# Performance work log

Hardware: AMD Instinct MI355X
Metric: run time of the kernel (lower is better)

Reference implementation:

```python
import jax, jax.numpy as jnp
import numpy as np

NINP = 768
HEAD = 12
ATTN_DIM = 768
PROT_DIM = 1024
B, T, S = 4, 2048, 512
EPS = 1e-5


def _lin_params(key, d_in, d_out):
    k1, k2 = jax.random.split(key)
    lim = 1.0 / np.sqrt(d_in)
    W = jax.random.uniform(k1, (d_in, d_out), jnp.float32, -lim, lim)
    b = jax.random.uniform(k2, (d_out,), jnp.float32, -lim, lim)
    return W, b


def setup_inputs() -> dict:
    key = jax.random.key(0)
    ks = jax.random.split(key, 16)
    x = jax.random.normal(ks[0], (B, T, NINP), jnp.float32)
    enc = jax.random.normal(ks[1], (B, S, PROT_DIM), jnp.float32)
    sWq, sbq = _lin_params(ks[2], NINP, ATTN_DIM)
    sWk, sbk = _lin_params(ks[3], NINP, ATTN_DIM)
    sWv, sbv = _lin_params(ks[4], NINP, ATTN_DIM)
    sWo, sbo = _lin_params(ks[5], ATTN_DIM, NINP)
    cWq, cbq = _lin_params(ks[6], NINP, ATTN_DIM)
    cWk, cbk = _lin_params(ks[7], PROT_DIM, ATTN_DIM)
    cWv, cbv = _lin_params(ks[8], PROT_DIM, ATTN_DIM)
    cWo, cbo = _lin_params(ks[9], ATTN_DIM, NINP)
    mW1, mb1 = _lin_params(ks[10], NINP, 4 * NINP)
    mW2, mb2 = _lin_params(ks[11], 4 * NINP, NINP)
    return dict(
        x=x, encoder_hidden_states=enc,
        ln1_g=jnp.ones((NINP,)), ln1_b=jnp.zeros((NINP,)),
        ln2_g=jnp.ones((NINP,)), ln2_b=jnp.zeros((NINP,)),
        sWq=sWq, sbq=sbq, sWk=sWk, sbk=sbk, sWv=sWv, sbv=sbv, sWo=sWo, sbo=sbo,
        cWq=cWq, cbq=cbq, cWk=cWk, cbk=cbk, cWv=cWv, cbv=cbv, cWo=cWo, cbo=cbo,
        mW1=mW1, mb1=mb1, mW2=mW2, mb2=mb2,
    )


def _ln(x, g, b):
    mu = jnp.mean(x, -1, keepdims=True)
    var = jnp.mean(jnp.square(x - mu), -1, keepdims=True)
    return (x - mu) * jax.lax.rsqrt(var + EPS) * g + b


def _attn(xq, xkv, Wq, bq, Wk, bk, Wv, bv, Wo, bo, causal):
    Bq, Tq, _ = xq.shape
    Sk = xkv.shape[1]
    hd = ATTN_DIM // HEAD
    q = (xq @ Wq + bq).reshape(Bq, Tq, HEAD, hd).transpose(0, 2, 1, 3)
    k = (xkv @ Wk + bk).reshape(Bq, Sk, HEAD, hd).transpose(0, 2, 1, 3)
    v = (xkv @ Wv + bv).reshape(Bq, Sk, HEAD, hd).transpose(0, 2, 1, 3)
    att = jnp.einsum('bhtd,bhsd->bhts', q, k) * (1.0 / np.sqrt(hd))
    if causal:
        mask = jnp.tril(jnp.ones((Tq, Sk), bool))
        att = jnp.where(mask, att, -jnp.inf)
    att = jax.nn.softmax(att, axis=-1)
    y = jnp.einsum('bhts,bhsd->bhtd', att, v)
    y = y.transpose(0, 2, 1, 3).reshape(Bq, Tq, ATTN_DIM)
    return y @ Wo + bo


def reference(x, encoder_hidden_states, ln1_g, ln1_b, ln2_g, ln2_b,
              sWq, sbq, sWk, sbk, sWv, sbv, sWo, sbo,
              cWq, cbq, cWk, cbk, cWv, cbv, cWo, cbo,
              mW1, mb1, mW2, mb2):
    # NOTE: original code does x = ln1(x), so the residual adds onto the
    # NORMED input (faithful to source quirk). is_causal=True, multi_mode=True.
    xn = _ln(x, ln1_g, ln1_b)
    x = xn + _attn(xn, xn, sWq, sbq, sWk, sbk, sWv, sbv, sWo, sbo, causal=True)
    x = x + _attn(x, encoder_hidden_states, cWq, cbq, cWk, cbk, cWv, cbv, cWo, cbo, causal=False)
    h = _ln(x, ln2_g, ln2_b)
    h = jax.nn.gelu(h @ mW1 + mb1, approximate=False) @ mW2 + mb2
    return x + h
```

## Files before the change

kernel.cpp:

```cpp
#include <hip/hip_runtime.h>
#include <math.h>

typedef unsigned short u16;
typedef __attribute__((ext_vector_type(8))) short short8;
typedef __attribute__((ext_vector_type(4))) short bf16x4;
typedef __attribute__((ext_vector_type(4))) float f32x4;

static __device__ __forceinline__ u16 f2bf(float f) {
    union { float f; unsigned int u; } c; c.f = f;
    unsigned int u = c.u;
    u += 0x7FFF + ((u >> 16) & 1);
    return (u16)(u >> 16);
}
static __device__ __forceinline__ float bf2f(u16 u) {
    union { unsigned int i; float f; } c; c.i = ((unsigned int)u) << 16;
    return c.f;
}
static __device__ __forceinline__ float gelu_f(float v) {
    float y = 0.7978845608f * (v + 0.044715f * v * v * v);
    return v / (1.0f + __expf(-2.0f * y));
}

#define GLOAD16(g, s) __builtin_amdgcn_global_load_lds( \
    (const __attribute__((address_space(1))) void*)(g), \
    (__attribute__((address_space(3))) void*)(s), 16, 0, 0)

struct PrepArgs {
    const float* src[11];
    u16* dst[11];
    int K[11];
    int N[11];
    int end[11];
    int cnt;
};

__global__ void k_prep(PrepArgs a)
{
    __shared__ float tile[32][33];
    const int bid = blockIdx.x;
    int e = 0;
    while (e < a.cnt - 1 && bid >= a.end[e]) e++;
    const int local = bid - (e ? a.end[e - 1] : 0);
    const float* __restrict__ src = a.src[e];
    u16* __restrict__ dst = a.dst[e];
    const int K = a.K[e], N = a.N[e];
    const int tx = threadIdx.x, ty = threadIdx.y;

    if (K == 0) {
        size_t base = (size_t)local * 2048 + (size_t)(ty * 32 + tx) * 8;
        float4 v0 = *(const float4*)(src + base);
        float4 v1 = *(const float4*)(src + base + 4);
        short8 o;
        o[0] = (short)f2bf(v0.x); o[1] = (short)f2bf(v0.y);
        o[2] = (short)f2bf(v0.z); o[3] = (short)f2bf(v0.w);
        o[4] = (short)f2bf(v1.x); o[5] = (short)f2bf(v1.y);
        o[6] = (short)f2bf(v1.z); o[7] = (short)f2bf(v1.w);
        *(short8*)&dst[base] = o;
        return;
    }
    const int nbx = N / 32;
    const int bx = local % nbx, by = local / nbx;
    const int n0 = bx * 32, k0 = by * 32;
#pragma unroll
    for (int i = 0; i < 4; i++)
        tile[ty + i * 8][tx] = src[(size_t)(k0 + ty + i * 8) * N + n0 + tx];
    __syncthreads();
#pragma unroll
    for (int i = 0; i < 4; i++)
        dst[(size_t)(n0 + ty + i * 8) * K + k0 + tx] = f2bf(tile[tx][ty + i * 8]);
}

__global__ __launch_bounds__(256) void k_layernorm(
    const float* __restrict__ x, const float* __restrict__ g, const float* __restrict__ b,
    float* __restrict__ outF, u16* __restrict__ outB)
{
    const int row = blockIdx.x, t = threadIdx.x;
    const float* xr = x + (size_t)row * 768;
    float v[3];
#pragma unroll
    for (int i = 0; i < 3; i++) v[i] = xr[t + i * 256];
    __shared__ float sred[4];
    float s = v[0] + v[1] + v[2];
#pragma unroll
    for (int o = 32; o; o >>= 1) s += __shfl_xor(s, o, 64);
    if ((t & 63) == 0) sred[t >> 6] = s;
    __syncthreads();
    float mu = (sred[0] + sred[1] + sred[2] + sred[3]) * (1.0f / 768.0f);
    __syncthreads();
    float q = 0.f;
#pragma unroll
    for (int i = 0; i < 3; i++) { float d = v[i] - mu; q += d * d; }
#pragma unroll
    for (int o = 32; o; o >>= 1) q += __shfl_xor(q, o, 64);
    if ((t & 63) == 0) sred[t >> 6] = q;
    __syncthreads();
    float var = (sred[0] + sred[1] + sred[2] + sred[3]) * (1.0f / 768.0f);
    float rstd = rsqrtf(var + 1e-5f);
#pragma unroll
    for (int i = 0; i < 3; i++) {
        int c = t + i * 256;
        float y = (v[i] - mu) * rstd * g[c] + b[c];
        if (outF) outF[(size_t)row * 768 + c] = y;
        if (outB) outB[(size_t)row * 768 + c] = f2bf(y);
    }
}

template<int BN>
__global__ __launch_bounds__(256) void k_gemm(
    const u16* __restrict__ A, const u16* __restrict__ Bt,
    const float* __restrict__ b1, const float* __restrict__ b2, const float* __restrict__ b3,
    const float* __restrict__ resid,
    float* __restrict__ outF, u16* __restrict__ outB, u16* __restrict__ outK, u16* __restrict__ outV,
    int M, int N, int K, int do_gelu, int mode, int vT_log)
{
    constexpr int MR = (BN == 128) ? 4 : 2;
    __shared__ u16 As[128 * 32];
    __shared__ u16 Bs[BN * 32];
    const int t = threadIdx.x;
    const int w = t >> 6, l = t & 63;
    const int lr = l & 15, lg = l >> 4;

    const unsigned nwg = gridDim.x * gridDim.y;
    unsigned bid = blockIdx.y * gridDim.x + blockIdx.x;
    bid = (bid & 7) * (nwg >> 3) + (bid >> 3);
    const int m0 = (bid / gridDim.x) * 128, n0 = (bid % gridDim.x) * BN;

    const int wr = (BN == 128) ? ((w >> 1) * 64) : (w * 32);
    const int wc = (BN == 128) ? ((w & 1) * 64) : 0;

    const int srow = t >> 2;
    const int skk = (t & 3) * 8;
    const u16* ga0 = A + (size_t)(m0 + srow) * K + skk;
    const u16* ga1 = A + (size_t)(m0 + 64 + srow) * K + skk;
    const u16* gb0 = Bt + (size_t)(n0 + srow) * K + skk;
    const u16* gb1 = (BN == 128) ? (Bt + (size_t)(n0 + 64 + srow) * K + skk) : nullptr;
    u16* lA0 = &As[w * 512];
    u16* lA1 = &As[2048 + w * 512];
    u16* lB0 = &Bs[w * 512];
    u16* lB1 = (BN == 128) ? &Bs[2048 + w * 512] : nullptr;

    f32x4 acc[MR][4] = {};

    for (int k0 = 0; k0 < K; k0 += 32) {
        __syncthreads();
        GLOAD16(ga0 + k0, lA0);
        GLOAD16(ga1 + k0, lA1);
        GLOAD16(gb0 + k0, lB0);
        if (BN == 128) GLOAD16(gb1 + k0, lB1);
        __syncthreads();
        short8 af[MR], bfr[4];
#pragma unroll
        for (int m = 0; m < MR; m++) af[m] = *(const short8*)&As[(wr + m * 16 + lr) * 32 + lg * 8];
#pragma unroll
        for (int n = 0; n < 4; n++) bfr[n] = *(const short8*)&Bs[(wc + n * 16 + lr) * 32 + lg * 8];
#pragma unroll
        for (int m = 0; m < MR; m++)
#pragma unroll
            for (int n = 0; n < 4; n++)
                acc[m][n] = __builtin_amdgcn_mfma_f32_16x16x32_bf16(af[m], bfr[n], acc[m][n], 0, 0, 0);
    }

#pragma unroll
    for (int m = 0; m < MR; m++) {
        int row0 = m0 + wr + m * 16 + lg * 4;
#pragma unroll
        for (int n = 0; n < 4; n++) {
            int col = n0 + wc + n * 16 + lr;
            const float* bp = b1; int lc = col; u16* tgt = outB; int vT = 0;
            if (mode == 2) {
                if (col >= 1536)     { bp = b3; lc = col - 1536; tgt = outV; vT = 1; }
                else if (col >= 768) { bp = b2; lc = col - 768;  tgt = outK; }
            } else if (mode == 3) {
                if (col >= 768)      { bp = b3; lc = col - 768;  tgt = outV; vT = 1; }
            }
            float bv = bp[lc];
            float vv[4];
#pragma unroll
            for (int j = 0; j < 4; j++) {
                float v = acc[m][n][j] + bv;
                if (do_gelu) v = gelu_f(v);
                vv[j] = v;
            }
            if (mode == 0) {
#pragma unroll
                for (int j = 0; j < 4; j++) {
                    size_t idx = (size_t)(row0 + j) * N + col;
                    float v = vv[j];
                    if (resid) v += resid[idx];
                    if (outF) outF[idx] = v;
                    if (outB) outB[idx] = f2bf(v);
                }
            } else if (!vT) {
#pragma unroll
                for (int j = 0; j < 4; j++)
                    tgt[(size_t)(row0 + j) * 768 + lc] = f2bf(vv[j]);
            } else {
                int head = lc >> 6, d = lc & 63;
                int bq = row0 >> vT_log, s = row0 & ((1 << vT_log) - 1);
                bf16x4 pk;
#pragma unroll
                for (int j = 0; j < 4; j++) pk[j] = (short)f2bf(vv[j]);
                *(bf16x4*)&tgt[((size_t)((bq * 12 + head) * 64 + d) << vT_log) + s] = pk;
            }
        }
    }
}

template<bool CAUSAL>
__global__ __launch_bounds__(256) void k_attn(
    const u16* __restrict__ Q, const u16* __restrict__ K,
    const u16* __restrict__ Vt, u16* __restrict__ Y,
    int Tq, int Skv)
{
    const int bh = blockIdx.x;
    const int b = bh / 12, h = bh % 12;
    const int qt = CAUSAL ? ((int)gridDim.y - 1 - (int)blockIdx.y) : blockIdx.y;
    const int q0 = qt * 128;
    const int t = threadIdx.x, w = t >> 6, l = t & 63;
    const int lr = l & 15, lg = l >> 4;
    const int swz = (lr & 7) << 3;
    const float QSC = 0.125f * 1.44269504088896f;

    const u16* Qb = Q + (size_t)b * Tq * 768 + h * 64;
    const u16* Kb = K + (size_t)b * Skv * 768 + h * 64;
    const u16* Vb = Vt + (size_t)bh * 64 * Skv;

    __shared__ u16 Ks[2][64 * 64];
    __shared__ u16 Vs[2][64 * 64];
    __shared__ u16 Ps[4][32 * 64];

    short8 aq[2][2];
#pragma unroll
    for (int qn = 0; qn < 2; qn++) {
        const u16* qr = Qb + (size_t)(q0 + w * 32 + qn * 16 + lr) * 768 + lg * 8;
#pragma unroll
        for (int hh = 0; hh < 2; hh++) {
            short8 raw = *(const short8*)(qr + hh * 32);
            short8 sc;
#pragma unroll
            for (int i = 0; i < 8; i++) sc[i] = (short)f2bf(bf2f((u16)raw[i]) * QSC);
            aq[qn][hh] = sc;
        }
    }

    f32x4 acc[2][4] = {};
    float mrun[2] = { -INFINITY, -INFINITY };
    float lrun[2] = { 0.f, 0.f };

    const int nt = CAUSAL ? (2 * qt + 2) : (Skv / 64);

    const int r0 = t >> 3, r1 = 32 + (t >> 3);
    const int db = (t & 7) * 8;
    const int sw0 = db ^ ((r0 & 7) << 3);
    const int sw1 = db ^ ((r1 & 7) << 3);

    short8 kr0, kr1, vr0, vr1;
    kr0 = *(const short8*)(Kb + (size_t)r0 * 768 + db);
    kr1 = *(const short8*)(Kb + (size_t)r1 * 768 + db);
    vr0 = *(const short8*)(Vb + (size_t)r0 * Skv + db);
    vr1 = *(const short8*)(Vb + (size_t)r1 * Skv + db);
    *(short8*)&Ks[0][r0 * 64 + sw0] = kr0;
    *(short8*)&Ks[0][r1 * 64 + sw1] = kr1;
    *(short8*)&Vs[0][r0 * 64 + sw0] = vr0;
    *(short8*)&Vs[0][r1 * 64 + sw1] = vr1;
    __syncthreads();
    int cur = 0;

    for (int kt = 0; kt < nt; kt++) {
        const int kv0 = kt * 64;
        const bool more = (kt + 1 < nt);
        if (more) {
            const int kn = kv0 + 64;
            kr0 = *(const short8*)(Kb + (size_t)(kn + r0) * 768 + db);
            kr1 = *(const short8*)(Kb + (size_t)(kn + r1) * 768 + db);
            vr0 = *(const short8*)(Vb + (size_t)r0 * Skv + kn + db);
            vr1 = *(const short8*)(Vb + (size_t)r1 * Skv + kn + db);
        }

        const u16* KsC = Ks[cur];
        f32x4 st[2][4];
        __builtin_amdgcn_s_setprio(1);
#pragma unroll
        for (int c = 0; c < 4; c++) {
            const short8 kb0 = *(const short8*)&KsC[(c * 16 + lr) * 64 + ((lg * 8) ^ swz)];
            const short8 kb1 = *(const short8*)&KsC[(c * 16 + lr) * 64 + ((32 | (lg * 8)) ^ swz)];
#pragma unroll
            for (int qn = 0; qn < 2; qn++) {
                f32x4 a = {};
                a = __builtin_amdgcn_mfma_f32_16x16x32_bf16(kb0, aq[qn][0], a, 0, 0, 0);
                a = __builtin_amdgcn_mfma_f32_16x16x32_bf16(kb1, aq[qn][1], a, 0, 0, 0);
                st[qn][c] = a;
            }
        }
        __builtin_amdgcn_s_setprio(0);

        if (CAUSAL && kt >= nt - 2) {
#pragma unroll
            for (int qn = 0; qn < 2; qn++) {
                int qv = q0 + w * 32 + qn * 16 + lr;
#pragma unroll
                for (int c = 0; c < 4; c++)
#pragma unroll
                    for (int j = 0; j < 4; j++) {
                        int kvv = kv0 + c * 16 + lg * 4 + j;
                        if (kvv > qv) st[qn][c][j] = -1e30f;
                    }
            }
        }

        float mv[2];
#pragma unroll
        for (int qn = 0; qn < 2; qn++) {
            float m = st[qn][0][0];
#pragma unroll
            for (int c = 0; c < 4; c++)
#pragma unroll
                for (int j = 0; j < 4; j++) m = fmaxf(m, st[qn][c][j]);
            m = fmaxf(m, __shfl_xor(m, 16, 64));
            m = fmaxf(m, __shfl_xor(m, 32, 64));
            mv[qn] = m;
        }
        float need = fmaxf(mv[0] - mrun[0], mv[1] - mrun[1]);
        if (!__all(need <= 8.0f)) {
#pragma unroll
            for (int qn = 0; qn < 2; qn++) {
                float mnew = fmaxf(mrun[qn], mv[qn]);
                float sc = exp2f(mrun[qn] - mnew);
                mrun[qn] = mnew;
                lrun[qn] *= sc;
#pragma unroll
                for (int c = 0; c < 4; c++)
#pragma unroll
                    for (int j = 0; j < 4; j++) acc[qn][c][j] *= sc;
            }
        }
        u16* pw = Ps[w];
#pragma unroll
        for (int qn = 0; qn < 2; qn++) {
            float r = 0.f;
#pragma unroll
            for (int c = 0; c < 4; c++)
#pragma unroll
                for (int j = 0; j < 4; j++) {
                    float p = exp2f(st[qn][c][j] - mrun[qn]);
                    st[qn][c][j] = p;
                    r += p;
                }
            r += __shfl_xor(r, 16, 64);
            r += __shfl_xor(r, 32, 64);
            lrun[qn] += r;
            const int prow = qn * 16 + lr;
#pragma unroll
            for (int c = 0; c < 4; c++) {
                bf16x4 pk;
#pragma unroll
                for (int j = 0; j < 4; j++) pk[j] = (short)f2bf(st[qn][c][j]);
                *(bf16x4*)&pw[prow * 64 + ((c * 16 + lg * 4) ^ swz)] = pk;
            }
        }

        const u16* VsC = Vs[cur];
        __builtin_amdgcn_s_setprio(1);
#pragma unroll
        for (int qn = 0; qn < 2; qn++) {
            const short8 pb0 = *(const short8*)&pw[(qn * 16 + lr) * 64 + ((lg * 8) ^ swz)];
            const short8 pb1 = *(const short8*)&pw[(qn * 16 + lr) * 64 + ((32 | (lg * 8)) ^ swz)];
#pragma unroll
            for (int c = 0; c < 4; c++) {
                const short8 vb0 = *(const short8*)&VsC[(c * 16 + lr) * 64 + ((lg * 8) ^ swz)];
                const short8 vb1 = *(const short8*)&VsC[(c * 16 + lr) * 64 + ((32 | (lg * 8)) ^ swz)];
                acc[qn][c] = __builtin_amdgcn_mfma_f32_16x16x32_bf16(vb0, pb0, acc[qn][c], 0, 0, 0);
                acc[qn][c] = __builtin_amdgcn_mfma_f32_16x16x32_bf16(vb1, pb1, acc[qn][c], 0, 0, 0);
            }
        }
        __builtin_amdgcn_s_setprio(0);

        if (more) {
            *(short8*)&Ks[cur ^ 1][r0 * 64 + sw0] = kr0;
            *(short8*)&Ks[cur ^ 1][r1 * 64 + sw1] = kr1;
            *(short8*)&Vs[cur ^ 1][r0 * 64 + sw0] = vr0;
            *(short8*)&Vs[cur ^ 1][r1 * 64 + sw1] = vr1;
            __syncthreads();
            cur ^= 1;
        }
    }

#pragma unroll
    for (int qn = 0; qn < 2; qn++) {
        float inv = 1.0f / lrun[qn];
        int q = q0 + w * 32 + qn * 16 + lr;
        size_t yb = (size_t)(b * Tq + q) * 768 + h * 64;
#pragma unroll
        for (int c = 0; c < 4; c++) {
            bf16x4 pk;
#pragma unroll
            for (int j = 0; j < 4; j++) pk[j] = (short)f2bf(acc[qn][c][j] * inv);
            *(bf16x4*)&Y[yb + c * 16 + lg * 4] = pk;
        }
    }
}

extern "C" void kernel_launch(void* const* d_in, const int* in_sizes, int n_in,
                              void* d_out, int out_size, void* d_ws, size_t ws_size,
                              hipStream_t stream)
{
    (void)in_sizes; (void)n_in; (void)out_size; (void)ws_size;
    const float* x    = (const float*)d_in[0];
    const float* enc  = (const float*)d_in[1];
    const float* ln1g = (const float*)d_in[2];
    const float* ln1b = (const float*)d_in[3];
    const float* ln2g = (const float*)d_in[4];
    const float* ln2b = (const float*)d_in[5];
    const float* sWq  = (const float*)d_in[6];
    const float* sbq  = (const float*)d_in[7];
    const float* sWk  = (const float*)d_in[8];
    const float* sbk  = (const float*)d_in[9];
    const float* sWv  = (const float*)d_in[10];
    const float* sbv  = (const float*)d_in[11];
    const float* sWo  = (const float*)d_in[12];
    const float* sbo  = (const float*)d_in[13];
    const float* cWq  = (const float*)d_in[14];
    const float* cbq  = (const float*)d_in[15];
    const float* cWk  = (const float*)d_in[16];
    const float* cbk  = (const float*)d_in[17];
    const float* cWv  = (const float*)d_in[18];
    const float* cbv  = (const float*)d_in[19];
    const float* cWo  = (const float*)d_in[20];
    const float* cbo  = (const float*)d_in[21];
    const float* mW1  = (const float*)d_in[22];
    const float* mb1  = (const float*)d_in[23];
    const float* mW2  = (const float*)d_in[24];
    const float* mb2  = (const float*)d_in[25];
    float* out = (float*)d_out;

    const int Bb = 4, T = 2048, S = 512, C = 768, P = 1024, F = 3072;
    const int M = Bb * T;
    const int MS = Bb * S;

    char* ws = (char*)d_ws;
    size_t off = 0;
    auto alloc = [&](size_t bytes) -> void* {
        void* p = ws + off;
        off += (bytes + 255) & ~(size_t)255;
        return p;
    };

    u16* wqkvT = (u16*)alloc((size_t)3 * C * C * 2);
    u16* sWoT  = (u16*)alloc((size_t)C * C * 2);
    u16* cWqT  = (u16*)alloc((size_t)C * C * 2);
    u16* ckvT  = (u16*)alloc((size_t)2 * C * P * 2);
    u16* cWoT  = (u16*)alloc((size_t)C * C * 2);
    u16* mW1T  = (u16*)alloc((size_t)F * C * 2);
    u16* mW2T  = (u16*)alloc((size_t)C * F * 2);
    u16* encbf = (u16*)alloc((size_t)MS * P * 2);
    float* slotA = (float*)alloc((size_t)M * C * 4);
    float* slotB = (float*)alloc((size_t)M * C * 4);
    u16*   slotC = (u16*)alloc((size_t)M * C * 2);
    u16*   big   = (u16*)alloc((size_t)M * F * 2);

    u16* qbf = big;
    u16* kbf = big + (size_t)M * C;
    u16* vbf = big + (size_t)2 * M * C;
    u16* ybf = big + (size_t)3 * M * C;
    u16* midbf = big;

    float* xn = slotA;
    float* x2 = slotA;
    float* x1 = slotB;
    u16* xbf = slotC;

    PrepArgs pa;
    const float* srcs[11] = { sWq, sWk, sWv, sWo, cWq, cWk, cWv, cWo, mW1, mW2, enc };
    u16* dsts[11] = { wqkvT, wqkvT + (size_t)C * C, wqkvT + (size_t)2 * C * C,
                      sWoT, cWqT, ckvT, ckvT + (size_t)C * P, cWoT, mW1T, mW2T, encbf };
    int Ks_[11] = { C, C, C, C, C, P, P, C, C, F, 0 };
    int Ns_[11] = { C, C, C, C, C, C, C, C, F, C, MS * P };
    int cum = 0;
    for (int i = 0; i < 11; i++) {
        pa.src[i] = srcs[i]; pa.dst[i] = dsts[i]; pa.K[i] = Ks_[i]; pa.N[i] = Ns_[i];
        int nb = Ks_[i] ? (Ns_[i] / 32) * (Ks_[i] / 32) : (Ns_[i] / 2048);
        cum += nb; pa.end[i] = cum;
    }
    pa.cnt = 11;
    k_prep<<<cum, dim3(32, 8), 0, stream>>>(pa);

    k_layernorm<<<M, 256, 0, stream>>>(x, ln1g, ln1b, xn, xbf);

    k_gemm<128><<<dim3(18, 64), 256, 0, stream>>>(
        xbf, wqkvT, sbq, sbk, sbv, nullptr, nullptr, qbf, kbf, vbf, M, 2304, C, 0, 2, 11);

    k_attn<true><<<dim3(Bb * 12, T / 128), 256, 0, stream>>>(qbf, kbf, vbf, ybf, T, T);

    k_gemm<64><<<dim3(12, 64), 256, 0, stream>>>(
        ybf, sWoT, sbo, nullptr, nullptr, xn, x1, xbf, nullptr, nullptr, M, C, C, 0, 0, 0);

    k_gemm<64><<<dim3(12, 64), 256, 0, stream>>>(
        xbf, cWqT, cbq, nullptr, nullptr, nullptr, nullptr, qbf, nullptr, nullptr, M, C, C, 0, 0, 0);

    k_gemm<64><<<dim3(24, 16), 256, 0, stream>>>(
        encbf, ckvT, cbk, nullptr, cbv, nullptr, nullptr, kbf, nullptr, vbf, MS, 1536, P, 0, 3, 9);

    k_attn<false><<<dim3(Bb * 12, T / 128), 256, 0, stream>>>(qbf, kbf, vbf, ybf, T, S);

    k_gemm<64><<<dim3(12, 64), 256, 0, stream>>>(
        ybf, cWoT, cbo, nullptr, nullptr, x1, x2, nullptr, nullptr, nullptr, M, C, C, 0, 0, 0);

    k_layernorm<<<M, 256, 0, stream>>>(x2, ln2g, ln2b, nullptr, xbf);

    k_gemm<128><<<dim3(24, 64), 256, 0, stream>>>(
        xbf, mW1T, mb1, nullptr, nullptr, nullptr, nullptr, midbf, nullptr, nullptr, M, F, C, 1, 0, 0);

    k_gemm<64><<<dim3(12, 64), 256, 0, stream>>>(
        midbf, mW2T, mb2, nullptr, nullptr, x2, out, nullptr, nullptr, nullptr, M, C, F, 0, 0, 0);
}
```

Measured before the change: 466.0 us.

## Double GEMM K-tile to 64 with XOR-swizzled LDS layout

The GEMM kernel now stages a 64-wide K slice per iteration instead of 32, which halves the number of barrier pairs per K loop. The shared-memory tiles are stored with an XOR swizzle on 16-byte slots, applied on the global-to-LDS load side and undone on the fragment reads, to avoid LDS bank conflicts. In exchange LDS use doubles, which may lower occupancy, and there is still no double buffering, so loads and MFMA work do not overlap.

```diff
diff --git a/kernel.cpp b/kernel.cpp
--- a/kernel.cpp
+++ b/kernel.cpp
@@ -114,8 +114,8 @@
     int M, int N, int K, int do_gelu, int mode, int vT_log)
 {
     constexpr int MR = (BN == 128) ? 4 : 2;
-    __shared__ u16 As[128 * 32];
-    __shared__ u16 Bs[BN * 32];
+    __shared__ u16 As[128 * 64];
+    __shared__ u16 Bs[BN * 64];
     const int t = threadIdx.x;
     const int w = t >> 6, l = t & 63;
     const int lr = l & 15, lg = l >> 4;
@@ -128,36 +128,46 @@
     const int wr = (BN == 128) ? ((w >> 1) * 64) : (w * 32);
     const int wc = (BN == 128) ? ((w & 1) * 64) : 0;
 
-    const int srow = t >> 2;
-    const int skk = (t & 3) * 8;
-    const u16* ga0 = A + (size_t)(m0 + srow) * K + skk;
-    const u16* ga1 = A + (size_t)(m0 + 64 + srow) * K + skk;
-    const u16* gb0 = Bt + (size_t)(n0 + srow) * K + skk;
-    const u16* gb1 = (BN == 128) ? (Bt + (size_t)(n0 + 64 + srow) * K + skk) : nullptr;
-    u16* lA0 = &As[w * 512];
-    u16* lA1 = &As[2048 + w * 512];
-    u16* lB0 = &Bs[w * 512];
-    u16* lB1 = (BN == 128) ? &Bs[2048 + w * 512] : nullptr;
+    const int srow = t >> 3;
+    const int sslot = t & 7;
 
     f32x4 acc[MR][4] = {};
 
-    for (int k0 = 0; k0 < K; k0 += 32) {
+    for (int k0 = 0; k0 < K; k0 += 64) {
         __syncthreads();
-        GLOAD16(ga0 + k0, lA0);
-        GLOAD16(ga1 + k0, lA1);
-        GLOAD16(gb0 + k0, lB0);
-        if (BN == 128) GLOAD16(gb1 + k0, lB1);
+#pragma unroll
+        for (int i = 0; i < 4; i++) {
+            int row = i * 32 + srow;
+            GLOAD16(A + (size_t)(m0 + row) * K + k0 + ((sslot ^ (row & 7)) * 8),
+                    &As[i * 2048 + w * 512]);
+        }
+#pragma unroll
+        for (int i = 0; i < BN / 32; i++) {
+            int row = i * 32 + srow;
+            GLOAD16(Bt + (size_t)(n0 + row) * K + k0 + ((sslot ^ (row & 7)) * 8),
+                    &Bs[i * 2048 + w * 512]);
+        }
         __syncthreads();
-        short8 af[MR], bfr[4];
-#pragma unroll
-        for (int m = 0; m < MR; m++) af[m] = *(const short8*)&As[(wr + m * 16 + lr) * 32 + lg * 8];
-#pragma unroll
-        for (int n = 0; n < 4; n++) bfr[n] = *(const short8*)&Bs[(wc + n * 16 + lr) * 32 + lg * 8];
-#pragma unroll
-        for (int m = 0; m < MR; m++)
-#pragma unroll
-            for (int n = 0; n < 4; n++)
-                acc[m][n] = __builtin_amdgcn_mfma_f32_16x16x32_bf16(af[m], bfr[n], acc[m][n], 0, 0, 0);
+#pragma unroll
+        for (int kk = 0; kk < 2; kk++) {
+            const int ce = kk * 32 + lg * 8;
+            short8 af[MR], bfr[4];
+#pragma unroll
+            for (int m = 0; m < MR; m++) {
+                int row = wr + m * 16 + lr;
+                af[m] = *(const short8*)&As[row * 64 + (ce ^ ((row & 7) << 3))];
+            }
+#pragma unroll
+            for (int n = 0; n < 4; n++) {
+                int row = wc + n * 16 + lr;
+                bfr[n] = *(const short8*)&Bs[row * 64 + (ce ^ ((row & 7) << 3))];
+            }
+#pragma unroll
+            for (int m = 0; m < MR; m++)
+#pragma unroll
+                for (int n = 0; n < 4; n++)
+                    acc[m][n] = __builtin_amdgcn_mfma_f32_16x16x32_bf16(af[m], bfr[n], acc[m][n], 0, 0, 0);
+        }
     }
 
 #pragma unroll
```

Result: faster. 429.6 us (-7.8%).
